# Kernel tuning notes

Hardware: AMD Instinct MI355X
Metric: run time of the kernel (lower is better)

The kernel has to match this reference:

```python
import jax, jax.numpy as jnp
import numpy as np

D_MODEL = 512
N_HEADS = 8
NUM_NODES = 20
EPS = 1e-5

def _layer_norm(x, g, b):
    mu = jnp.mean(x, axis=-1, keepdims=True)
    var = jnp.var(x, axis=-1, keepdims=True)
    return (x - mu) * jax.lax.rsqrt(var + EPS) * g + b

def _conv1d(x_bcn, w_oik):
    # x: [B, C, N], w: [O, I, K], padding = K//2 (same)
    k = w_oik.shape[-1]
    p = k // 2
    return jax.lax.conv_general_dilated(
        x_bcn, w_oik, window_strides=(1,), padding=[(p, p)],
        dimension_numbers=('NCH', 'OIH', 'NCH'))

def setup_inputs() -> dict:
    key = jax.random.key(0)
    ks = jax.random.split(key, 6)
    B, N, D, H = 4096, NUM_NODES, D_MODEL, N_HEADS
    x = jax.random.normal(ks[0], (B, N, D), dtype=jnp.float32)
    s = 1.0 / np.sqrt(D * 3)
    Wq = jax.random.normal(ks[1], (D, D, 3), dtype=jnp.float32) * s
    Wk = jax.random.normal(ks[2], (D, D, 3), dtype=jnp.float32) * s
    Wv = jax.random.normal(ks[3], (D, D, 3), dtype=jnp.float32) * s
    rel_table = jax.random.normal(ks[4], (2 * N - 1, H), dtype=jnp.float32) * 0.02
    Wo = jax.random.normal(ks[5], (D, D), dtype=jnp.float32) * (1.0 / np.sqrt(D))
    bo = jnp.zeros((D,), dtype=jnp.float32)
    ones = jnp.ones((D,), dtype=jnp.float32)
    zeros = jnp.zeros((D,), dtype=jnp.float32)
    return {"x": x, "Wq": Wq, "Wk": Wk, "Wv": Wv,
            "lnq_g": ones, "lnq_b": zeros, "lnk_g": ones, "lnk_b": zeros,
            "lnv_g": ones, "lnv_b": zeros,
            "rel_table": rel_table, "Wo": Wo, "bo": bo}

def reference(x, Wq, Wk, Wv, lnq_g, lnq_b, lnk_g, lnk_b, lnv_g, lnv_b, rel_table, Wo, bo):
    B, N, D = x.shape
    H = N_HEADS
    dk = D // H
    x_p = jnp.transpose(x, (0, 2, 1))  # [B, D, N]

    def proj(W, g, b):
        c = _conv1d(x_p, W)                      # [B, D, N]
        c = _layer_norm(jnp.transpose(c, (0, 2, 1)), g, b)  # [B, N, D]
        return x + c                              # residual

    q = proj(Wq, lnq_g, lnq_b)
    k = proj(Wk, lnk_g, lnk_b)
    v = proj(Wv, lnv_g, lnv_b)

    q = q.reshape(B, N, H, dk).transpose(0, 2, 1, 3)  # [B,H,N,dk]
    k = k.reshape(B, N, H, dk).transpose(0, 2, 1, 3)
    v = v.reshape(B, N, H, dk).transpose(0, 2, 1, 3)

    scale = 1.0 / np.sqrt(dk)
    scores = jnp.einsum('bhnd,bhmd->bhnm', q, k) * scale  # [B,H,N,N]

    # relative position bias: index[i,j] = i - j + N - 1
    coords = jnp.arange(N)
    rel_idx = coords[:, None] - coords[None, :] + (N - 1)   # [N,N]
    rel_bias = rel_table[rel_idx]                            # [N,N,H]
    rel_bias = jnp.transpose(rel_bias, (2, 0, 1))[None]      # [1,H,N,N]
    scores = scores + rel_bias

    attn = jax.nn.softmax(scores, axis=-1)
    out = jnp.einsum('bhnm,bhmd->bhnd', attn, v)             # [B,H,N,dk]
    out = out.transpose(0, 2, 1, 3).reshape(B, N, D)
    return out @ Wo.T + bo
```

## Files before the change

kernel.cpp:

```cpp
#include <hip/hip_runtime.h>
#include <hip/hip_bf16.h>
#include <stdint.h>

typedef __attribute__((ext_vector_type(8))) __bf16 bf16x8;
typedef __attribute__((ext_vector_type(2))) __bf16 bf16x2;
typedef __attribute__((ext_vector_type(4))) float f32x4;

#define B_TOT   4096
#define NN      20
#define DM      512
#define NC1     1536
#define M_TOT   (B_TOT*NN)
#define NPAD    22

__device__ __forceinline__ void async_copy16(const __bf16* g, __bf16* l) {
    __builtin_amdgcn_global_load_lds(
        (__attribute__((address_space(1))) void*)g,
        (__attribute__((address_space(3))) void*)l, 16, 0, 0);
}

template<typename T>
__device__ __forceinline__ void load8(const T* p, float* r) {
    if constexpr (sizeof(T) == 4) {
        f32x4 a = *(const f32x4*)p;
        f32x4 b = *(const f32x4*)(p + 4);
#pragma unroll
        for (int i = 0; i < 4; ++i) { r[i] = a[i]; r[i + 4] = b[i]; }
    } else {
        bf16x8 a = *(const bf16x8*)p;
#pragma unroll
        for (int i = 0; i < 8; ++i) r[i] = (float)a[i];
    }
}

__global__ void detect_kernel(const uint32_t* __restrict__ xw, int* __restrict__ mode) {
    int lane = threadIdx.x & 63;
    int susp = 0;
#pragma unroll
    for (int i = 0; i < 4; ++i) {
        uint32_t w = xw[lane * 4 + i];
        uint32_t e = (w >> 7) & 0xFF;
        if ((e >= 118 && e <= 130) || (w & 0xFFFFu) == 0) susp++;
    }
#pragma unroll
    for (int o = 32; o > 0; o >>= 1) susp += __shfl_xor(susp, o, 64);
    if (lane == 0) *mode = (susp > 128) ? 1 : 0;
}

template<typename T>
__device__ __forceinline__ void wt_body(
    const T* __restrict__ Wq, const T* __restrict__ Wk, const T* __restrict__ Wv,
    const T* __restrict__ Wo, __bf16* __restrict__ Wt, __bf16* __restrict__ Wob, int t)
{
    if (t < 3 * 512 * 512) {
        int p = t >> 18;
        int r = t & 262143;
        int o = r >> 9, i = r & 511;
        const T* W = (p == 0) ? Wq : ((p == 1) ? Wk : Wv);
        const T* src = W + (size_t)(o * 512 + i) * 3;
        float w0 = (float)src[0], w1 = (float)src[1], w2 = (float)src[2];
        size_t base = (size_t)(p * 512 + o) * 1536 + i;
        Wt[base]        = (__bf16)w0;
        Wt[base + 512]  = (__bf16)w1;
        Wt[base + 1024] = (__bf16)w2;
    } else {
        int g2 = t - 3 * 512 * 512;
        Wob[g2] = (__bf16)(float)Wo[g2];
    }
}

__global__ __launch_bounds__(256) void wt_kernel(
    const void* Wq, const void* Wk, const void* Wv, const void* Wo,
    __bf16* Wt, __bf16* Wob, const int* mode)
{
    int t = blockIdx.x * 256 + threadIdx.x;
    if (*mode)
        wt_body<__bf16>((const __bf16*)Wq, (const __bf16*)Wk, (const __bf16*)Wv,
                        (const __bf16*)Wo, Wt, Wob, t);
    else
        wt_body<float>((const float*)Wq, (const float*)Wk, (const float*)Wv,
                       (const float*)Wo, Wt, Wob, t);
}

template<typename T>
__device__ __forceinline__ void xpad_body(
    const T* __restrict__ x, __bf16* __restrict__ xp, int idx)
{
    int col = (idx & 63) * 8;
    int row = idx >> 6;
    int b = row / 22;
    int np = row - b * 22;
    bf16x8 ov;
    if (np == 0 || np == 21) {
#pragma unroll
        for (int t = 0; t < 8; ++t) ov[t] = (__bf16)0.f;
    } else {
        float tmp[8];
        load8<T>(x + ((size_t)(b * 20 + np - 1) * 512 + col), tmp);
#pragma unroll
        for (int t = 0; t < 8; ++t) ov[t] = (__bf16)tmp[t];
    }
    *(bf16x8*)(xp + (size_t)row * 512 + col) = ov;
}

__global__ __launch_bounds__(256) void xpad_kernel(
    const void* x, __bf16* xp, const int* mode)
{
    int idx = blockIdx.x * 256 + threadIdx.x;
    if (*mode) xpad_body<__bf16>((const __bf16*)x, xp, idx);
    else       xpad_body<float>((const float*)x, xp, idx);
}

#define SBAR()  __builtin_amdgcn_s_barrier()
#define SCHED0() __builtin_amdgcn_sched_barrier(0)
#define LGKM0() do { asm volatile("s_waitcnt lgkmcnt(0)" ::: "memory"); SCHED0(); } while (0)
#define VM4()   do { SCHED0(); asm volatile("s_waitcnt vmcnt(4)" ::: "memory"); } while (0)
#define VM0()   do { SCHED0(); asm volatile("s_waitcnt vmcnt(0)" ::: "memory"); } while (0)

__device__ __forceinline__ void g1_loadA(const __bf16* slab, int off, bf16x8 (&aq)[4]) {
#pragma unroll
    for (int i = 0; i < 4; ++i) aq[i] = *(const bf16x8*)(slab + off + i * 512);
}
__device__ __forceinline__ void g1_loadB(const __bf16* slab, int off, bf16x8 (&bq)[4]) {
#pragma unroll
    for (int i = 0; i < 4; ++i) bq[i] = *(const bf16x8*)(slab + off + i * 512);
}
template<int QM>
__device__ __forceinline__ void g1_mma(bf16x8 (&aq)[4], bf16x8 (&bq)[4], f32x4 (&acc)[8][4]) {
    __builtin_amdgcn_s_setprio(1);
#pragma unroll
    for (int i = 0; i < 4; ++i)
#pragma unroll
        for (int nf = 0; nf < 4; ++nf)
            acc[QM * 4 + i][nf] = __builtin_amdgcn_mfma_f32_16x16x32_bf16(
                aq[i], bq[nf], acc[QM * 4 + i][nf], 0, 0, 0);
    __builtin_amdgcn_s_setprio(0);
}

__global__ __launch_bounds__(512, 2) void g1_kernel(
    const __bf16* __restrict__ xpad, const __bf16* __restrict__ Wt,
    __bf16* __restrict__ Cout, int mbase)
{
    extern __shared__ __align__(16) __bf16 sh[];
    __bf16* shA = sh;
    __bf16* shB = sh + 32768;

    const int tid = threadIdx.x;
    const int w = tid >> 6, l = tid & 63;
    const int lr = l & 15, lq = l >> 4;
    const int wm = w >> 2, wn = w & 3;

    int nwg = gridDim.x;
    int bid = blockIdx.x;
    if ((nwg & 7) == 0) bid = (bid & 7) * (nwg >> 3) + (bid >> 3);
    const int nb = bid % 6;
    const int mb = bid / 6;
    const int n0 = nb * 256;
    const int mloc = mb * 256;

    const int rin = l >> 2;
    const int pc  = (l & 3) * 8;
    const int lc  = (rin >= 8) ? (pc ^ 16) : pc;
    const int R0 = w * 16 + rin;
    const int R1 = 128 + R0;
    const int g0 = mbase + mloc + R0, g1r = mbase + mloc + R1;
    const __bf16* aP0 = xpad + (size_t)((g0 / 20) * 22 + g0 % 20) * 512 + lc;
    const __bf16* aP1 = xpad + (size_t)((g1r / 20) * 22 + g1r % 20) * 512 + lc;
    const __bf16* bP0 = Wt + (size_t)(n0 + R0) * 1536 + lc;
    const __bf16* bP1 = Wt + (size_t)(n0 + R1) * 1536 + lc;
    const int sdst = w * 512 + l * 8;

    const int swzcol = (lr >= 8) ? ((lq * 8) ^ 16) : (lq * 8);
    const int ardoff = lr * 32 + swzcol;
    const int rdA = wm * 8 * 512 + ardoff;
    const int rdB = wn * 4 * 512 + ardoff;

    f32x4 acc[8][4] = {};
    bf16x8 aq[4], bq[4];

    { __bf16* d = shA + 0 * 8192 + sdst; async_copy16(aP0 + 0, d);  async_copy16(aP1 + 0, d + 4096); }
    { __bf16* d = shB + 0 * 8192 + sdst; async_copy16(bP0 + 0, d);  async_copy16(bP1 + 0, d + 4096); }
    { __bf16* d = shA + 1 * 8192 + sdst; async_copy16(aP0 + 32, d); async_copy16(aP1 + 32, d + 4096); }
    { __bf16* d = shB + 1 * 8192 + sdst; async_copy16(bP0 + 32, d); async_copy16(bP1 + 32, d + 4096); }
    VM4();
    SBAR();

    for (int t = 0; t < 24; ++t) {
        const int cur = t & 1;
        const __bf16* A0 = shA + (cur * 2 + 0) * 8192;
        const __bf16* A1 = shA + (cur * 2 + 1) * 8192;
        const __bf16* B0 = shB + (cur * 2 + 0) * 8192;
        const __bf16* B1 = shB + (cur * 2 + 1) * 8192;
        __bf16* dA0 = shA + ((cur ^ 1) * 2 + 0) * 8192 + sdst;
        __bf16* dA1 = shA + ((cur ^ 1) * 2 + 1) * 8192 + sdst;
        __bf16* dB0 = shB + ((cur ^ 1) * 2 + 0) * 8192 + sdst;
        __bf16* dB1 = shB + ((cur ^ 1) * 2 + 1) * 8192 + sdst;
        const int kn = (t + 1) * 64;
        const bool st = (t < 23);

        g1_loadA(A0, rdA, aq);
        g1_loadB(B0, rdB, bq);
        if (st) { async_copy16(aP0 + kn, dA0); async_copy16(aP1 + kn, dA0 + 4096); }
        SBAR(); LGKM0();
        g1_mma<0>(aq, bq, acc);
        SBAR();

        g1_loadA(A0, rdA + 2048, aq);
        if (st) { async_copy16(bP0 + kn, dB0); async_copy16(bP1 + kn, dB0 + 4096); }
        if (st) VM4(); else VM0();
        SBAR(); LGKM0();
        g1_mma<1>(aq, bq, acc);
        SBAR();

        g1_loadA(A1, rdA, aq);
        g1_loadB(B1, rdB, bq);
        if (st) { async_copy16(aP0 + kn + 32, dA1); async_copy16(aP1 + kn + 32, dA1 + 4096); }
        SBAR(); LGKM0();
        g1_mma<0>(aq, bq, acc);
        SBAR();

        g1_loadA(A1, rdA + 2048, aq);
        if (st) { async_copy16(bP0 + kn + 32, dB1); async_copy16(bP1 + kn + 32, dB1 + 4096); }
        if (st) VM4();
        SBAR(); LGKM0();
        g1_mma<1>(aq, bq, acc);
        SBAR();
    }

#pragma unroll
    for (int mf = 0; mf < 8; ++mf) {
#pragma unroll
        for (int r = 0; r < 4; ++r) {
            int row = mloc + wm * 128 + mf * 16 + lq * 4 + r;
            size_t base = (size_t)row * 1536 + n0 + wn * 64 + lr;
#pragma unroll
            for (int nf = 0; nf < 4; ++nf)
                Cout[base + nf * 16] = (__bf16)acc[mf][nf][r];
        }
    }
}

template<typename T>
__device__ __forceinline__ void attn_body(
    const __bf16* __restrict__ xpad, const __bf16* __restrict__ cqkv,
    const T* __restrict__ lnq_g, const T* __restrict__ lnq_b,
    const T* __restrict__ lnk_g, const T* __restrict__ lnk_b,
    const T* __restrict__ lnv_g, const T* __restrict__ lnv_b,
    const T* __restrict__ rel, __bf16* __restrict__ aout, int bbase,
    __bf16* sq , float* S , float* rb )
{
    const int tid = threadIdx.x;
    const int wave = tid >> 6, lane = tid & 63;
    const int bl = blockIdx.x;
    const size_t xpbase = ((size_t)(bbase + bl) * NPAD + 1) * DM;
    const size_t cbase = (size_t)bl * NN * NC1;

    for (int t = tid; t < 312; t += 256) rb[t] = (float)rel[t];

    for (int rr = 0; rr < 15; ++rr) {
        int row = wave * 15 + rr;
        int p = row / 20;
        int n = row - p * 20;
        bf16x8 cv = *(const bf16x8*)(cqkv + cbase + (size_t)n * NC1 + p * 512 + lane * 8);
        float vals[8]; float s = 0.f, ss = 0.f;
#pragma unroll
        for (int t = 0; t < 8; ++t) { float f = (float)cv[t]; vals[t] = f; s += f; ss += f * f; }
#pragma unroll
        for (int o = 32; o > 0; o >>= 1) { s += __shfl_xor(s, o, 64); ss += __shfl_xor(ss, o, 64); }
        float mu = s * (1.f / 512.f);
        float var = ss * (1.f / 512.f) - mu * mu;
        float rs = rsqrtf(var + 1e-5f);
        const T* g  = (p == 0) ? lnq_g : (p == 1) ? lnk_g : lnv_g;
        const T* bb = (p == 0) ? lnq_b : (p == 1) ? lnk_b : lnv_b;
        float gv[8], bv[8];
        load8<T>(g  + lane * 8, gv);
        load8<T>(bb + lane * 8, bv);
        bf16x8 xv = *(const bf16x8*)(xpad + xpbase + (size_t)n * DM + lane * 8);
        bf16x8 ov;
#pragma unroll
        for (int t = 0; t < 8; ++t)
            ov[t] = (__bf16)((vals[t] - mu) * rs * gv[t] + bv[t] + (float)xv[t]);
        *(bf16x8*)(sq + ((size_t)p * 20 + n) * 512 + lane * 8) = ov;
    }
    __syncthreads();

    if (tid < 160) {
        int h = tid / 20, j = tid - (tid / 20) * 20;
        float kreg[64];
        const __bf16* kr = sq + (size_t)(1 * 20 + j) * 512 + h * 64;
#pragma unroll
        for (int t = 0; t < 64; t += 8) {
            bf16x8 kv = *(const bf16x8*)(kr + t);
#pragma unroll
            for (int u = 0; u < 8; ++u) kreg[t + u] = (float)kv[u];
        }
        for (int i = 0; i < 20; ++i) {
            const __bf16* qr = sq + (size_t)(0 * 20 + i) * 512 + h * 64;
            float s = 0.f;
#pragma unroll
            for (int t = 0; t < 64; t += 8) {
                bf16x8 qv = *(const bf16x8*)(qr + t);
#pragma unroll
                for (int u = 0; u < 8; ++u) s += (float)qv[u] * kreg[t + u];
            }
            S[(h * 20 + i) * 20 + j] = s * 0.125f + rb[(i - j + 19) * 8 + h];
        }
    }
    __syncthreads();

    if (tid < 160) {
        int h = tid / 20, i = tid - (tid / 20) * 20;
        float* row = &S[(h * 20 + i) * 20];
        float mx = row[0];
        for (int j = 1; j < 20; ++j) mx = fmaxf(mx, row[j]);
        float e[20]; float sum = 0.f;
        for (int j = 0; j < 20; ++j) { e[j] = expf(row[j] - mx); sum += e[j]; }
        float inv = 1.f / sum;
        for (int j = 0; j < 20; ++j) row[j] = e[j] * inv;
    }
    __syncthreads();

    {
        int h = tid >> 5;
        int d2 = (tid & 31) * 2;
        float v0[20], v1[20];
#pragma unroll
        for (int j = 0; j < 20; ++j) {
            const __bf16* vr = sq + (size_t)(2 * 20 + j) * 512 + h * 64 + d2;
            v0[j] = (float)vr[0]; v1[j] = (float)vr[1];
        }
        for (int i = 0; i < 20; ++i) {
            float o0 = 0.f, o1 = 0.f;
#pragma unroll
            for (int j = 0; j < 20; ++j) {
                float p = S[(h * 20 + i) * 20 + j];
                o0 += p * v0[j]; o1 += p * v1[j];
            }
            bf16x2 pr; pr[0] = (__bf16)o0; pr[1] = (__bf16)o1;
            *(bf16x2*)(sq + (size_t)i * 512 + h * 64 + d2) = pr;
        }
    }
    __syncthreads();

    {
        __bf16* ab = aout + (size_t)bl * NN * DM;
#pragma unroll
        for (int e = 0; e < 5; ++e) {
            int off = e * 2048 + tid * 8;
            *(bf16x8*)(ab + off) = *(const bf16x8*)(sq + off);
        }
    }
}

__global__ __launch_bounds__(256) void attn_kernel(
    const __bf16* xpad, const __bf16* cqkv,
    const void* lnq_g, const void* lnq_b, const void* lnk_g, const void* lnk_b,
    const void* lnv_g, const void* lnv_b, const void* rel,
    __bf16* aout, int bbase, const int* mode)
{
    __shared__ __align__(16) __bf16 sq[3 * 20 * 512];
    __shared__ float S[8 * 20 * 20];
    __shared__ float rb[320];
    if (*mode)
        attn_body<__bf16>(xpad, cqkv,
            (const __bf16*)lnq_g, (const __bf16*)lnq_b, (const __bf16*)lnk_g,
            (const __bf16*)lnk_b, (const __bf16*)lnv_g, (const __bf16*)lnv_b,
            (const __bf16*)rel, aout, bbase, sq, S, rb);
    else
        attn_body<float>(xpad, cqkv,
            (const float*)lnq_g, (const float*)lnq_b, (const float*)lnk_g,
            (const float*)lnk_b, (const float*)lnv_g, (const float*)lnv_b,
            (const float*)rel, aout, bbase, sq, S, rb);
}

template<typename T>
__device__ __forceinline__ void g3_body(
    const __bf16* __restrict__ Ain, const __bf16* __restrict__ Wob,
    const T* __restrict__ bo, T* __restrict__ out, int mbase,
    __bf16* As, __bf16* Bs)
{
    const int tid  = threadIdx.x;
    const int wave = tid >> 6, lane = tid & 63;
    const int n0 = blockIdx.x * 128;
    const int m0 = blockIdx.y * 128;
    const int srow = lane >> 3;
    const int scol = (lane & 7) * 8;
    const int lr = lane & 15, lq = lane >> 4;
    const int wm = (wave >> 1) * 64, wn = (wave & 1) * 64;
    f32x4 acc[4][4] = {};

    for (int kt = 0; kt < 8; ++kt) {
        const int k0 = kt * 64;
        __syncthreads();
#pragma unroll
        for (int j = 0; j < 4; ++j) {
            int rb_ = wave * 32 + j * 8;
            async_copy16(Ain + (size_t)(m0 + rb_ + srow) * 512 + (k0 + scol),
                         As + rb_ * 64 + lane * 8);
            async_copy16(Wob + (size_t)(n0 + rb_ + srow) * 512 + (k0 + scol),
                         Bs + rb_ * 64 + lane * 8);
        }
        __syncthreads();
#pragma unroll
        for (int ko = 0; ko < 64; ko += 32) {
            bf16x8 af[4], bfv[4];
#pragma unroll
            for (int mi = 0; mi < 4; ++mi)
                af[mi] = *(const bf16x8*)&As[(wm + mi * 16 + lr) * 64 + ko + lq * 8];
#pragma unroll
            for (int ni = 0; ni < 4; ++ni)
                bfv[ni] = *(const bf16x8*)&Bs[(wn + ni * 16 + lr) * 64 + ko + lq * 8];
#pragma unroll
            for (int mi = 0; mi < 4; ++mi)
#pragma unroll
                for (int ni = 0; ni < 4; ++ni)
                    acc[mi][ni] = __builtin_amdgcn_mfma_f32_16x16x32_bf16(
                        af[mi], bfv[ni], acc[mi][ni], 0, 0, 0);
        }
    }
#pragma unroll
    for (int mi = 0; mi < 4; ++mi) {
#pragma unroll
        for (int r = 0; r < 4; ++r) {
            int row = m0 + wm + mi * 16 + lq * 4 + r;
            size_t gbase = (size_t)(mbase + row) * 512 + n0 + wn + lr;
#pragma unroll
            for (int ni = 0; ni < 4; ++ni) {
                float bias = (float)bo[n0 + wn + lr + ni * 16];
                out[gbase + ni * 16] = (T)(acc[mi][ni][r] + bias);
            }
        }
    }
}

__global__ __launch_bounds__(256) void g3_kernel(
    const __bf16* Ain, const __bf16* Wob, const void* bo, void* out,
    int mbase, const int* mode)
{
    __shared__ __align__(16) __bf16 As[128 * 64];
    __shared__ __align__(16) __bf16 Bs[128 * 64];
    if (*mode) g3_body<__bf16>(Ain, Wob, (const __bf16*)bo, (__bf16*)out, mbase, As, Bs);
    else       g3_body<float>(Ain, Wob, (const float*)bo, (float*)out, mbase, As, Bs);
}

extern "C" void kernel_launch(void* const* d_in, const int* in_sizes, int n_in,
                              void* d_out, int out_size, void* d_ws, size_t ws_size,
                              hipStream_t stream) {
    (void)in_sizes; (void)n_in; (void)out_size;
    char* ws = (char*)d_ws;
    int*    mode = (int*)ws;
    __bf16* Wt   = (__bf16*)(ws + 256);
    __bf16* Wob  = (__bf16*)(ws + 256 + 4718592);
    __bf16* xpad = (__bf16*)(ws + 256 + 4718592 + 524288);
    const size_t off_c = 256 + 4718592 + 524288 + (size_t)B_TOT * NPAD * DM * 2;

    static bool attr_set = false;
    if (!attr_set) {
        (void)hipFuncSetAttribute((const void*)g1_kernel,
                                  hipFuncAttributeMaxDynamicSharedMemorySize, 131072);
        attr_set = true;
    }

    int CH = 4;
    while (CH < 64) {
        size_t rows = (size_t)M_TOT / CH;
        if (off_c + rows * (size_t)NC1 * 2 + rows * (size_t)DM * 2 <= ws_size) break;
        CH *= 2;
    }
    const int rows = M_TOT / CH;
    const int Bc   = B_TOT / CH;
    __bf16* Cbuf = (__bf16*)(ws + off_c);
    __bf16* Abuf = (__bf16*)(ws + off_c + (size_t)rows * NC1 * 2);

    detect_kernel<<<dim3(1), dim3(64), 0, stream>>>((const uint32_t*)d_in[0], mode);
    wt_kernel<<<dim3(4096), dim3(256), 0, stream>>>(
        d_in[1], d_in[2], d_in[3], d_in[11], Wt, Wob, mode);
    xpad_kernel<<<dim3(22528), dim3(256), 0, stream>>>(d_in[0], xpad, mode);

    for (int c = 0; c < CH; ++c) {
        int mbase = c * rows;
        g1_kernel<<<dim3(6 * (rows / 256)), dim3(512), 131072, stream>>>(
            xpad, Wt, Cbuf, mbase);
        attn_kernel<<<dim3(Bc), dim3(256), 0, stream>>>(
            xpad, Cbuf, d_in[4], d_in[5], d_in[6], d_in[7], d_in[8], d_in[9],
            d_in[10], Abuf, mbase / NN, mode);
        g3_kernel<<<dim3(4, rows / 128), dim3(256), 0, stream>>>(
            Abuf, Wob, d_in[12], d_out, mbase, mode);
    }
}
```

Measured before the change: 1.006 ms.

## Compute attention scores and PV with MFMA, swizzled LDS, 512-thread blocks

The per-batch attention kernel now uses 32x32x16 bf16 MFMA instructions for QK^T and P·V, one wave per head. The scalar per-thread dot products and the shared score matrix are gone, and softmax runs in registers with a cross-half shuffle. The Q/K/V staging in LDS gets an XOR swizzle to avoid bank conflicts. Blocks grow to 512 threads, and the chunk count now starts at 1 so fewer, larger launches run when workspace permits. Costs: padding 20x20 up to 32x32 wastes MFMA work, and the scalar gather of V bf16 elements may be slow.

```diff
diff --git a/kernel.cpp b/kernel.cpp
--- a/kernel.cpp
+++ b/kernel.cpp
@@ -1,10 +1,12 @@
 #include <hip/hip_runtime.h>
 #include <hip/hip_bf16.h>
 #include <stdint.h>
+#include <string.h>
 
 typedef __attribute__((ext_vector_type(8))) __bf16 bf16x8;
 typedef __attribute__((ext_vector_type(2))) __bf16 bf16x2;
 typedef __attribute__((ext_vector_type(4))) float f32x4;
+typedef __attribute__((ext_vector_type(16))) float f32x16;
 
 #define B_TOT   4096
 #define NN      20
@@ -31,6 +33,26 @@
 #pragma unroll
         for (int i = 0; i < 8; ++i) r[i] = (float)a[i];
     }
+}
+
+__device__ __forceinline__ bf16x8 zero8() {
+    bf16x8 z;
+#pragma unroll
+    for (int i = 0; i < 8; ++i) z[i] = (__bf16)0.f;
+    return z;
+}
+
+__device__ __forceinline__ uint32_t pkbf(float a, float b) {
+    __bf16 x = (__bf16)a, y = (__bf16)b;
+    uint16_t ux, uy;
+    __builtin_memcpy(&ux, &x, 2); __builtin_memcpy(&uy, &y, 2);
+    return (uint32_t)ux | ((uint32_t)uy << 16);
+}
+
+__device__ __forceinline__ bf16x8 mkfrag(uint32_t w0, uint32_t w1, uint32_t w2, uint32_t w3) {
+    union { uint32_t u[4]; bf16x8 v; } X;
+    X.u[0] = w0; X.u[1] = w1; X.u[2] = w2; X.u[3] = w3;
+    return X.v;
 }
 
 __global__ void detect_kernel(const uint32_t* __restrict__ xw, int* __restrict__ mode) {
@@ -92,8 +114,7 @@
     int np = row - b * 22;
     bf16x8 ov;
     if (np == 0 || np == 21) {
-#pragma unroll
-        for (int t = 0; t < 8; ++t) ov[t] = (__bf16)0.f;
+        ov = zero8();
     } else {
         float tmp[8];
         load8<T>(x + ((size_t)(b * 20 + np - 1) * 512 + col), tmp);
@@ -247,18 +268,21 @@
     const T* __restrict__ lnk_g, const T* __restrict__ lnk_b,
     const T* __restrict__ lnv_g, const T* __restrict__ lnv_b,
     const T* __restrict__ rel, __bf16* __restrict__ aout, int bbase,
-    __bf16* sq , float* S , float* rb )
+    __bf16* sq , float* rbt )
 {
     const int tid = threadIdx.x;
     const int wave = tid >> 6, lane = tid & 63;
     const int bl = blockIdx.x;
+    char* sqb = (char*)sq;
     const size_t xpbase = ((size_t)(bbase + bl) * NPAD + 1) * DM;
     const size_t cbase = (size_t)bl * NN * NC1;
 
-    for (int t = tid; t < 312; t += 256) rb[t] = (float)rel[t];
-
-    for (int rr = 0; rr < 15; ++rr) {
-        int row = wave * 15 + rr;
+    for (int t = tid; t < 312; t += 512) {
+        int h = t & 7, d = t >> 3;
+        rbt[h * 40 + d] = (float)rel[t];
+    }
+
+    for (int row = wave; row < 60; row += 8) {
         int p = row / 20;
         int n = row - p * 20;
         bf16x8 cv = *(const bf16x8*)(cqkv + cbase + (size_t)n * NC1 + p * 512 + lane * 8);
@@ -280,97 +304,126 @@
 #pragma unroll
         for (int t = 0; t < 8; ++t)
             ov[t] = (__bf16)((vals[t] - mu) * rs * gv[t] + bv[t] + (float)xv[t]);
-        *(bf16x8*)(sq + ((size_t)p * 20 + n) * 512 + lane * 8) = ov;
+        *(bf16x8*)(sqb + row * 1024 + ((lane * 16) ^ ((row & 7) << 4))) = ov;
     }
     __syncthreads();
 
-    if (tid < 160) {
-        int h = tid / 20, j = tid - (tid / 20) * 20;
-        float kreg[64];
-        const __bf16* kr = sq + (size_t)(1 * 20 + j) * 512 + h * 64;
-#pragma unroll
-        for (int t = 0; t < 64; t += 8) {
-            bf16x8 kv = *(const bf16x8*)(kr + t);
-#pragma unroll
-            for (int u = 0; u < 8; ++u) kreg[t + u] = (float)kv[u];
-        }
-        for (int i = 0; i < 20; ++i) {
-            const __bf16* qr = sq + (size_t)(0 * 20 + i) * 512 + h * 64;
-            float s = 0.f;
-#pragma unroll
-            for (int t = 0; t < 64; t += 8) {
-                bf16x8 qv = *(const bf16x8*)(qr + t);
-#pragma unroll
-                for (int u = 0; u < 8; ++u) s += (float)qv[u] * kreg[t + u];
+    const int h  = wave;
+    const int ic = lane & 31;
+    const int lq = lane >> 5;
+
+    f32x16 s;
+#pragma unroll
+    for (int r = 0; r < 16; ++r) s[r] = 0.f;
+#pragma unroll
+    for (int call = 0; call < 4; ++call) {
+        int kb2 = (call * 16 + lq * 8) * 2;
+        bf16x8 af = zero8(), bf_ = zero8();
+        if (ic < 20) {
+            int rk = 20 + ic;
+            af  = *(const bf16x8*)(sqb + rk * 1024 + ((h * 128 + kb2) ^ ((rk & 7) << 4)));
+            bf_ = *(const bf16x8*)(sqb + ic * 1024 + ((h * 128 + kb2) ^ ((ic & 7) << 4)));
+        }
+        s = __builtin_amdgcn_mfma_f32_32x32x16_bf16(af, bf_, s, 0, 0, 0);
+    }
+    __syncthreads();
+
+    float p_[16];
+    float mx = -1e30f;
+#pragma unroll
+    for (int r = 0; r < 16; ++r) {
+        int j = (r & 3) + 8 * (r >> 2) + 4 * lq;
+        if (j < 20) {
+            int d = ic - j + 19;
+            d = d < 0 ? 0 : (d > 38 ? 38 : d);
+            float v = s[r] * 0.125f + rbt[h * 40 + d];
+            p_[r] = v;
+            mx = fmaxf(mx, v);
+        } else p_[r] = -1e30f;
+    }
+    mx = fmaxf(mx, __shfl_xor(mx, 32, 64));
+    float sum = 0.f;
+#pragma unroll
+    for (int r = 0; r < 16; ++r) {
+        int j = (r & 3) + 8 * (r >> 2) + 4 * lq;
+        float e = (j < 20) ? expf(p_[r] - mx) : 0.f;
+        p_[r] = e; sum += e;
+    }
+    sum += __shfl_xor(sum, 32, 64);
+    float inv = 1.f / sum;
+#pragma unroll
+    for (int r = 0; r < 16; ++r) p_[r] *= inv;
+
+    uint32_t pk[8], qk[8];
+#pragma unroll
+    for (int k = 0; k < 8; ++k) pk[k] = pkbf(p_[2 * k], p_[2 * k + 1]);
+#pragma unroll
+    for (int k = 0; k < 8; ++k) qk[k] = (uint32_t)__shfl_xor((int)pk[k], 32, 64);
+    bf16x8 pa1 = lq ? mkfrag(qk[2], qk[3], pk[2], pk[3]) : mkfrag(pk[0], pk[1], qk[0], qk[1]);
+    bf16x8 pa2 = lq ? mkfrag(qk[6], qk[7], pk[6], pk[7]) : mkfrag(pk[4], pk[5], qk[4], qk[5]);
+
+#pragma unroll
+    for (int half = 0; half < 2; ++half) {
+        f32x16 o;
+#pragma unroll
+        for (int r = 0; r < 16; ++r) o[r] = 0.f;
+        const int cb2 = h * 128 + half * 64 + ic * 2;
+#pragma unroll
+        for (int call = 0; call < 2; ++call) {
+            int jb = call * 16 + lq * 8;
+            union { unsigned short u[8]; bf16x8 v; } V;
+#pragma unroll
+            for (int e = 0; e < 8; ++e) {
+                int j = jb + e;
+                unsigned short val = 0;
+                if (j < 20) {
+                    int rv = 40 + j;
+                    val = *(const unsigned short*)(sqb + rv * 1024 + (cb2 ^ ((rv & 7) << 4)));
+                }
+                V.u[e] = val;
             }
-            S[(h * 20 + i) * 20 + j] = s * 0.125f + rb[(i - j + 19) * 8 + h];
+            o = __builtin_amdgcn_mfma_f32_32x32x16_bf16(call ? pa2 : pa1, V.v, o, 0, 0, 0);
+        }
+#pragma unroll
+        for (int r = 0; r < 16; ++r) {
+            int i = (r & 3) + 8 * (r >> 2) + 4 * lq;
+            if (i < 20) {
+                __bf16 b = (__bf16)o[r];
+                unsigned short ub;
+                __builtin_memcpy(&ub, &b, 2);
+                *(unsigned short*)(sqb + i * 1024 + (cb2 ^ ((i & 7) << 4))) = ub;
+            }
         }
     }
     __syncthreads();
 
-    if (tid < 160) {
-        int h = tid / 20, i = tid - (tid / 20) * 20;
-        float* row = &S[(h * 20 + i) * 20];
-        float mx = row[0];
-        for (int j = 1; j < 20; ++j) mx = fmaxf(mx, row[j]);
-        float e[20]; float sum = 0.f;
-        for (int j = 0; j < 20; ++j) { e[j] = expf(row[j] - mx); sum += e[j]; }
-        float inv = 1.f / sum;
-        for (int j = 0; j < 20; ++j) row[j] = e[j] * inv;
-    }
-    __syncthreads();
-
-    {
-        int h = tid >> 5;
-        int d2 = (tid & 31) * 2;
-        float v0[20], v1[20];
-#pragma unroll
-        for (int j = 0; j < 20; ++j) {
-            const __bf16* vr = sq + (size_t)(2 * 20 + j) * 512 + h * 64 + d2;
-            v0[j] = (float)vr[0]; v1[j] = (float)vr[1];
-        }
-        for (int i = 0; i < 20; ++i) {
-            float o0 = 0.f, o1 = 0.f;
-#pragma unroll
-            for (int j = 0; j < 20; ++j) {
-                float p = S[(h * 20 + i) * 20 + j];
-                o0 += p * v0[j]; o1 += p * v1[j];
-            }
-            bf16x2 pr; pr[0] = (__bf16)o0; pr[1] = (__bf16)o1;
-            *(bf16x2*)(sq + (size_t)i * 512 + h * 64 + d2) = pr;
-        }
-    }
-    __syncthreads();
-
-    {
-        __bf16* ab = aout + (size_t)bl * NN * DM;
-#pragma unroll
-        for (int e = 0; e < 5; ++e) {
-            int off = e * 2048 + tid * 8;
-            *(bf16x8*)(ab + off) = *(const bf16x8*)(sq + off);
-        }
-    }
-}
-
-__global__ __launch_bounds__(256) void attn_kernel(
+    __bf16* ab = aout + (size_t)bl * NN * DM;
+    for (int t = tid; t < 1280; t += 512) {
+        int row = t >> 6;
+        int bc = (t & 63) * 16;
+        bf16x8 vv = *(const bf16x8*)(sqb + row * 1024 + (bc ^ ((row & 7) << 4)));
+        *(bf16x8*)(ab + t * 8) = vv;
+    }
+}
+
+__global__ __launch_bounds__(512) void attn_kernel(
     const __bf16* xpad, const __bf16* cqkv,
     const void* lnq_g, const void* lnq_b, const void* lnk_g, const void* lnk_b,
     const void* lnv_g, const void* lnv_b, const void* rel,
     __bf16* aout, int bbase, const int* mode)
 {
-    __shared__ __align__(16) __bf16 sq[3 * 20 * 512];
-    __shared__ float S[8 * 20 * 20];
-    __shared__ float rb[320];
+    __shared__ __align__(16) __bf16 sq[60 * 512];
+    __shared__ float rbt[8 * 40];
     if (*mode)
         attn_body<__bf16>(xpad, cqkv,
             (const __bf16*)lnq_g, (const __bf16*)lnq_b, (const __bf16*)lnk_g,
             (const __bf16*)lnk_b, (const __bf16*)lnv_g, (const __bf16*)lnv_b,
-            (const __bf16*)rel, aout, bbase, sq, S, rb);
+            (const __bf16*)rel, aout, bbase, sq, rbt);
     else
         attn_body<float>(xpad, cqkv,
             (const float*)lnq_g, (const float*)lnq_b, (const float*)lnk_g,
             (const float*)lnk_b, (const float*)lnv_g, (const float*)lnv_b,
-            (const float*)rel, aout, bbase, sq, S, rb);
+            (const float*)rel, aout, bbase, sq, rbt);
 }
 
 template<typename T>
@@ -461,7 +514,7 @@
         attr_set = true;
     }
 
-    int CH = 4;
+    int CH = 1;
     while (CH < 64) {
         size_t rows = (size_t)M_TOT / CH;
         if (off_c + rows * (size_t)NC1 * 2 + rows * (size_t)DM * 2 <= ws_size) break;
@@ -481,7 +534,7 @@
         int mbase = c * rows;
         g1_kernel<<<dim3(6 * (rows / 256)), dim3(512), 131072, stream>>>(
             xpad, Wt, Cbuf, mbase);
-        attn_kernel<<<dim3(Bc), dim3(256), 0, stream>>>(
+        attn_kernel<<<dim3(Bc), dim3(512), 0, stream>>>(
             xpad, Cbuf, d_in[4], d_in[5], d_in[6], d_in[7], d_in[8], d_in[9],
             d_in[10], Abuf, mbase / NN, mode);
         g3_kernel<<<dim3(4, rows / 128), dim3(256), 0, stream>>>(
```

Measured after the change: 857.2 us. -14.8%, faster.
